# Performance work log

Measured on AMD Instinct MI355X. Metric: run time of the kernel, lower is better.

## Reference

```python
import jax, jax.numpy as jnp
import numpy as np

CUBE_SIZE = 24
N_NEURONS = CUBE_SIZE ** 3  # 13824
INPUT_DIM = 512
OUTPUT_DIM = 1000
MAX_STEPS = 30
BATCH = 256


def _build_neighbor_indices(size: int) -> np.ndarray:
    """[N, 27] int32; invalid (out-of-cube) neighbors map to pad slot N."""
    n = size ** 3
    c = np.arange(size)
    z, y, x = np.meshgrid(c, c, c, indexing='ij')  # each [size,size,size]
    cols = []
    for dz in (-1, 0, 1):
        for dy in (-1, 0, 1):
            for dx in (-1, 0, 1):
                nz, ny, nx = z + dz, y + dy, x + dx
                valid = ((nz >= 0) & (nz < size) & (ny >= 0) & (ny < size)
                         & (nx >= 0) & (nx < size))
                idx = nz * size * size + ny * size + nx
                cols.append(np.where(valid, idx, n))
    return np.stack(cols, axis=-1).reshape(n, 27).astype(np.int32)


def setup_inputs() -> dict:
    key = jax.random.key(0)
    ks = jax.random.split(key, 4)
    # xavier-ish small init scales (gain 0.5 style)
    w_in = jax.random.normal(ks[0], (N_NEURONS, INPUT_DIM), jnp.float32) * 0.01
    w_local = jax.random.normal(ks[1], (N_NEURONS, 27), jnp.float32) * 0.1
    w_out = jax.random.normal(ks[2], (OUTPUT_DIM, N_NEURONS), jnp.float32) * 0.01
    x = jax.random.normal(ks[3], (BATCH, INPUT_DIM), jnp.float32)
    return {
        'x': x,
        'W_in_w': w_in,
        'W_in_b': jnp.zeros((N_NEURONS,), jnp.float32),
        'W_local': w_local,
        'W_out_w': w_out,
        'W_out_b': jnp.zeros((OUTPUT_DIM,), jnp.float32),
        'neighbor_indices': jnp.asarray(_build_neighbor_indices(CUBE_SIZE)),
    }


def reference(x, W_in_w, W_in_b, W_local, W_out_w, W_out_b, neighbor_indices):
    batch = x.shape[0]
    x_proj = x @ W_in_w.T + W_in_b  # [B, N]
    h0 = jnp.zeros((batch, N_NEURONS), x.dtype)
    pad = jnp.zeros((batch, 1), x.dtype)

    def step(h, _):
        h_padded = jnp.concatenate([h, pad], axis=1)        # [B, N+1]
        nbr = h_padded[:, neighbor_indices]                  # [B, N, 27]
        weighted = jnp.einsum('bnk,nk->bn', nbr, W_local)    # [B, N]
        return jnp.tanh(x_proj + weighted), None

    h, _ = jax.lax.scan(step, h0, None, length=MAX_STEPS)
    return h @ W_out_w.T + W_out_b  # [B, output_dim]
```

## Files before the change

kernel.cpp:

```cpp
#include <hip/hip_runtime.h>
#include <hip/hip_bf16.h>

#define NN   13824
#define BB   256
#define KDIM 512
#define ODIM 1000
#define CUBE 24
#define KS   16
#define XSTR 516
#define OSTR 452

typedef short bf8 __attribute__((ext_vector_type(8)));
typedef float f32x4 __attribute__((ext_vector_type(4)));

__device__ __forceinline__ float fast_tanh(float a) {
    float e = __expf(2.0f * a);
    return 1.0f - 2.0f / (e + 1.0f);
}
__device__ __forceinline__ float bf_lo(unsigned u) { return __uint_as_float(u << 16); }
__device__ __forceinline__ float bf_hi(unsigned u) { return __uint_as_float(u & 0xffff0000u); }
__device__ __forceinline__ unsigned short bf_rne(float f) {
    unsigned u = __float_as_uint(f);
    u += 0x7fffu + ((u >> 16) & 1u);
    return (unsigned short)(u >> 16);
}
__device__ __forceinline__ unsigned pk_bf16(float lo, float hi) {
    union { __hip_bfloat162 h; unsigned u; } cv;
    cv.h = __float22bfloat162_rn(make_float2(lo, hi));
    return cv.u;
}

__global__ __launch_bounds__(256) void xbf_kernel(
    const float* __restrict__ x, unsigned* __restrict__ xb)
{
    int i = blockIdx.x * 256 + threadIdx.x;
    float2 v = *(const float2*)&x[(size_t)i * 2];
    xb[i] = pk_bf16(v.x, v.y);
}

__global__ __launch_bounds__(256) void xproj_mfma(
    const float* __restrict__ w_in, const float* __restrict__ bias,
    const short* __restrict__ xbf, unsigned short* __restrict__ xp,
    unsigned short* __restrict__ h1)
{
    __shared__ unsigned short As[16 * XSTR];
    const int tid = threadIdx.x, w = tid >> 6, lane = tid & 63;
    const int quad = lane >> 4, l16 = lane & 15;
    const int n0 = blockIdx.x * 16;

#pragma unroll
    for (int rr = 0; rr < 4; ++rr) {
        const int row = w * 4 + rr;
        const float* __restrict__ src = &w_in[(size_t)(n0 + row) * KDIM];
#pragma unroll
        for (int c = 0; c < 2; ++c) {
            const int col = c * 256 + lane * 4;
            float4 v = *(const float4*)&src[col];
            uint2 pk2 = make_uint2(pk_bf16(v.x, v.y), pk_bf16(v.z, v.w));
            *(uint2*)&As[row * XSTR + col] = pk2;
        }
    }
    __syncthreads();

    f32x4 acc[4] = {};

    int ka = quad * 8;
    bf8 bb[4];
#pragma unroll
    for (int j = 0; j < 4; ++j)
        bb[j] = *(const bf8*)&xbf[(size_t)(w * 64 + j * 16 + l16) * KDIM + ka];

    for (int it = 0; it < 16; ++it) {
        bf8 nb[4] = {};
        if (it < 15) {
            const int nka = ka + 32;
#pragma unroll
            for (int j = 0; j < 4; ++j)
                nb[j] = *(const bf8*)&xbf[(size_t)(w * 64 + j * 16 + l16) * KDIM + nka];
        }
        bf8 af = *(const bf8*)&As[l16 * XSTR + it * 32 + quad * 8];
#pragma unroll
        for (int j = 0; j < 4; ++j)
            acc[j] = __builtin_amdgcn_mfma_f32_16x16x32_bf16(af, bb[j], acc[j], 0, 0, 0);
#pragma unroll
        for (int j = 0; j < 4; ++j) bb[j] = nb[j];
        ka += 32;
    }

#pragma unroll
    for (int j = 0; j < 4; ++j) {
        const int b = w * 64 + j * 16 + l16;
#pragma unroll
        for (int r = 0; r < 4; ++r) {
            const int n = n0 + quad * 4 + r;
            const float v = acc[j][r] + bias[n];
            xp[(size_t)n * BB + b] = bf_rne(v);
            h1[(size_t)n * BB + b] = bf_rne(fast_tanh(v));
        }
    }
}

__device__ __forceinline__ void load_plane_f2(
    const unsigned* __restrict__ h32, int z, int y, int xx, int dof, float2* w9)
{
#pragma unroll
    for (int j = 0; j < 9; ++j) {
        const int dz = j / 3 - 1, dy = j % 3 - 1;
        const int zz = z + dz, yy = y + dy;
        const bool valid = (xx >= 0) & (xx < CUBE) & (zz >= 0) & (zz < CUBE) &
                           (yy >= 0) & (yy < CUBE);
        unsigned v = 0u;
        if (valid) v = h32[(size_t)((zz * 24 + yy) * 24 + xx) * 128 + dof];
        w9[j] = make_float2(bf_lo(v), bf_hi(v));
    }
}

__global__ __launch_bounds__(256) void step_kernel(
    const unsigned* __restrict__ hprev, const unsigned* __restrict__ xp,
    const float* __restrict__ wl, unsigned* __restrict__ hnext)
{
    const int tid  = threadIdx.x;
    const int wid  = __builtin_amdgcn_readfirstlane(tid >> 6);
    const int wvb  = wid & 1;
    const int yoff = wid >> 1;
    const int lane = tid & 63;

    const int bid   = blockIdx.x;
    const int zhi   = bid & 7;
    const int inner = bid >> 3;
    const int yp    = inner % 12;
    const int r     = inner / 12;
    const int xc    = r & 3;
    const int zlo   = r >> 2;
    const int z     = zhi * 3 + zlo;
    const int y     = yp * 2 + yoff;

    const int x0   = xc * 6;
    const int dof  = wvb * 64 + lane;

    float2 win[5][9];
    load_plane_f2(hprev, z, y, x0 - 1, dof, win[0]);
    load_plane_f2(hprev, z, y, x0,     dof, win[1]);
    load_plane_f2(hprev, z, y, x0 + 1, dof, win[2]);
    load_plane_f2(hprev, z, y, x0 + 2, dof, win[3]);

#pragma unroll
    for (int xi = 0; xi < 6; ++xi) {
        const int x = x0 + xi;
        if (xi <= 3)
            load_plane_f2(hprev, z, y, x + 3, dof, win[(xi + 4) % 5]);

        const int n = (z * 24 + y) * 24 + x;
        const float* __restrict__ wn = &wl[(size_t)n * 27];
        const unsigned xpv = xp[(size_t)n * 128 + dof];
        float2 acc = make_float2(bf_lo(xpv), bf_hi(xpv));

        const float2* pm = win[xi % 5];
        const float2* pc = win[(xi + 1) % 5];
        const float2* pp = win[(xi + 2) % 5];
#pragma unroll
        for (int j = 0; j < 9; ++j) {
            const float w0 = wn[3 * j + 0];
            const float w1 = wn[3 * j + 1];
            const float w2 = wn[3 * j + 2];
            acc.x += w0 * pm[j].x + w1 * pc[j].x + w2 * pp[j].x;
            acc.y += w0 * pm[j].y + w1 * pc[j].y + w2 * pp[j].y;
        }
        hnext[(size_t)n * 128 + dof] = pk_bf16(fast_tanh(acc.x), fast_tanh(acc.y));
    }
}

__global__ __launch_bounds__(256) void transpose_kernel(
    const unsigned* __restrict__ h32, unsigned* __restrict__ hT32)
{
    __shared__ unsigned short T[64][66];
    const int tid = threadIdx.x;
    const int rr = tid >> 2, g = tid & 3;
    const int k0 = blockIdx.x * 64, b0 = blockIdx.y * 64;
#pragma unroll
    for (int i = 0; i < 8; ++i) {
        unsigned d = h32[(size_t)(k0 + rr) * 128 + b0 / 2 + g * 8 + i];
        const int bl = (g * 8 + i) * 2;
        T[bl][rr]     = (unsigned short)(d & 0xffffu);
        T[bl + 1][rr] = (unsigned short)(d >> 16);
    }
    __syncthreads();
#pragma unroll
    for (int i = 0; i < 8; ++i) {
        const int kl = (g * 8 + i) * 2;
        unsigned d = (unsigned)T[rr][kl] | ((unsigned)T[rr][kl + 1] << 16);
        hT32[(size_t)(b0 + rr) * (NN / 2) + k0 / 2 + g * 8 + i] = d;
    }
}

__global__ __launch_bounds__(512) void outgemm_mfma(
    const float* __restrict__ wout, const short* __restrict__ hT,
    float* __restrict__ part)
{
    __shared__ unsigned short As[128 * OSTR];
    const int tid = threadIdx.x, w = tid >> 6, lane = tid & 63;
    const int quad = lane >> 4, l16 = lane & 15;
    const int kb = blockIdx.x * (NN / KS);
    const int o0 = blockIdx.y * 128;
    const int b0 = blockIdx.z * 128 + w * 16;

    f32x4 acc[8] = {};

#pragma unroll 1
    for (int ph = 0; ph < 2; ++ph) {
        const int poff  = ph ? 448 : 0;
        const int pcols = ph ? 416 : 448;
        const int pkc   = ph ? 13 : 14;
        if (ph) __syncthreads();

#pragma unroll 4
        for (int rr = 0; rr < 16; ++rr) {
            const int row = w * 16 + rr;
            const int o = o0 + row;
            const float* __restrict__ src = &wout[(size_t)o * NN + kb + poff];
#pragma unroll
            for (int c = 0; c < 2; ++c) {
                const int col = c * 256 + lane * 4;
                if (col < pcols) {
                    float4 v = {0.f, 0.f, 0.f, 0.f};
                    if (o < ODIM) v = *(const float4*)&src[col];
                    *(uint2*)&As[row * OSTR + col] =
                        make_uint2(pk_bf16(v.x, v.y), pk_bf16(v.z, v.w));
                }
            }
        }
        __syncthreads();

        bf8 bb;
        {
            const int ka = kb + poff + quad * 8;
            bb = *(const bf8*)&hT[(size_t)(b0 + l16) * NN + ka];
        }
        for (int kc = 0; kc < pkc; ++kc) {
            bf8 nb = {};
            if (kc + 1 < pkc) {
                const int ka = kb + poff + (kc + 1) * 32 + quad * 8;
                nb = *(const bf8*)&hT[(size_t)(b0 + l16) * NN + ka];
            }
            const int cs = kc * 32 + quad * 8;
#pragma unroll
            for (int t = 0; t < 8; ++t) {
                bf8 af = *(const bf8*)&As[(t * 16 + l16) * OSTR + cs];
                acc[t] = __builtin_amdgcn_mfma_f32_16x16x32_bf16(af, bb, acc[t], 0, 0, 0);
            }
            bb = nb;
        }
    }

#pragma unroll
    for (int t = 0; t < 8; ++t) {
        const int b = b0 + l16;
#pragma unroll
        for (int r = 0; r < 4; ++r) {
            const int o = o0 + t * 16 + quad * 4 + r;
            part[((size_t)blockIdx.x * 1024 + o) * BB + b] = acc[t][r];
        }
    }
}

__global__ __launch_bounds__(256) void reduce_kernel(
    const float* __restrict__ part, const float* __restrict__ bias,
    float* __restrict__ out)
{
    const int o = blockIdx.x, b = threadIdx.x;
    float s = bias[o];
#pragma unroll
    for (int kc = 0; kc < KS; ++kc)
        s += part[((size_t)kc * 1024 + o) * BB + b];
    out[(size_t)b * ODIM + o] = s;
}

extern "C" void kernel_launch(void* const* d_in, const int* in_sizes, int n_in,
                              void* d_out, int out_size, void* d_ws, size_t ws_size,
                              hipStream_t stream)
{
    const float* x       = (const float*)d_in[0];
    const float* w_in    = (const float*)d_in[1];
    const float* b_in    = (const float*)d_in[2];
    const float* w_local = (const float*)d_in[3];
    const float* w_out   = (const float*)d_in[4];
    const float* b_out   = (const float*)d_in[5];
    float* out = (float*)d_out;

    char* p = (char*)d_ws;
    unsigned short* xp_bf = (unsigned short*)p;          p += (size_t)NN * BB * 2;
    unsigned short* hA    = (unsigned short*)p;          p += (size_t)NN * BB * 2;
    unsigned short* hB    = (unsigned short*)p;          p += (size_t)NN * BB * 2;
    unsigned short* hT    = (unsigned short*)p;          p += (size_t)NN * BB * 2;
    unsigned short* x_bf  = (unsigned short*)p;          p += (size_t)BB * KDIM * 2;
    float*          part  = (float*)p;

    xbf_kernel<<<256, 256, 0, stream>>>(x, (unsigned*)x_bf);
    xproj_mfma<<<864, 256, 0, stream>>>(w_in, b_in, (const short*)x_bf, xp_bf, hA);

    const unsigned* hp = (const unsigned*)hA;
    unsigned* hn = (unsigned*)hB;
    for (int s = 0; s < 29; ++s) {
        step_kernel<<<1152, 256, 0, stream>>>(hp, (const unsigned*)xp_bf, w_local, hn);
        unsigned* t = (unsigned*)hp; hp = hn; hn = t;
    }

    transpose_kernel<<<dim3(216, 4), 256, 0, stream>>>(hp, (unsigned*)hT);
    outgemm_mfma<<<dim3(KS, 8, 2), 512, 0, stream>>>(w_out, (const short*)hT, part);
    reduce_kernel<<<ODIM, 256, 0, stream>>>(part, b_out, out);
}
```

Measured before the change: 547.3 us.

## Retile step kernel to 4-wide x strips and double-buffer outgemm B loads

The stencil step kernel changes its thread-block decomposition. Each wave now handles its own y row, each thread walks 4 x positions instead of 6, and the grid grows to 1728 blocks. The input-projection values for all 4 positions are loaded up front to hide latency. The output GEMM gets a two-deep prefetch of the B fragments so global loads overlap more MFMA work. The trade-off is more parallelism and occupancy against more redundant halo-plane loads per output, since 6 planes are loaded per 4 outputs instead of 8 per 6.

```diff
diff --git a/kernel.cpp b/kernel.cpp
--- a/kernel.cpp
+++ b/kernel.cpp
@@ -121,22 +121,23 @@
 {
     const int tid  = threadIdx.x;
     const int wid  = __builtin_amdgcn_readfirstlane(tid >> 6);
-    const int wvb  = wid & 1;
-    const int yoff = wid >> 1;
     const int lane = tid & 63;
 
     const int bid   = blockIdx.x;
     const int zhi   = bid & 7;
     const int inner = bid >> 3;
-    const int yp    = inner % 12;
-    const int r     = inner / 12;
-    const int xc    = r & 3;
-    const int zlo   = r >> 2;
+    const int half  = inner & 1;
+    const int u     = inner >> 1;
+    const int xc    = u % 6;
+    const int u2    = u / 6;
+    const int yq    = u2 % 6;
+    const int zlo   = u2 / 6;
     const int z     = zhi * 3 + zlo;
-    const int y     = yp * 2 + yoff;
-
-    const int x0   = xc * 6;
-    const int dof  = wvb * 64 + lane;
+    const int y     = yq * 4 + wid;
+
+    const int x0   = xc * 4;
+    const int dof  = half * 64 + lane;
+    const int n0   = (z * 24 + y) * 24 + x0;
 
     float2 win[5][9];
     load_plane_f2(hprev, z, y, x0 - 1, dof, win[0]);
@@ -144,16 +145,20 @@
     load_plane_f2(hprev, z, y, x0 + 1, dof, win[2]);
     load_plane_f2(hprev, z, y, x0 + 2, dof, win[3]);
 
-#pragma unroll
-    for (int xi = 0; xi < 6; ++xi) {
+    unsigned xpv[4];
+#pragma unroll
+    for (int xi = 0; xi < 4; ++xi)
+        xpv[xi] = xp[(size_t)(n0 + xi) * 128 + dof];
+
+#pragma unroll
+    for (int xi = 0; xi < 4; ++xi) {
         const int x = x0 + xi;
-        if (xi <= 3)
+        if (xi <= 1)
             load_plane_f2(hprev, z, y, x + 3, dof, win[(xi + 4) % 5]);
 
-        const int n = (z * 24 + y) * 24 + x;
+        const int n = n0 + xi;
         const float* __restrict__ wn = &wl[(size_t)n * 27];
-        const unsigned xpv = xp[(size_t)n * 128 + dof];
-        float2 acc = make_float2(bf_lo(xpv), bf_hi(xpv));
+        float2 acc = make_float2(bf_lo(xpv[xi]), bf_hi(xpv[xi]));
 
         const float2* pm = win[xi % 5];
         const float2* pc = win[(xi + 1) % 5];
@@ -203,6 +208,8 @@
     const int kb = blockIdx.x * (NN / KS);
     const int o0 = blockIdx.y * 128;
     const int b0 = blockIdx.z * 128 + w * 16;
+
+    const short* __restrict__ brow = &hT[(size_t)(b0 + l16) * NN];
 
     f32x4 acc[8] = {};
 
@@ -231,24 +238,31 @@
         }
         __syncthreads();
 
-        bf8 bb;
-        {
-            const int ka = kb + poff + quad * 8;
-            bb = *(const bf8*)&hT[(size_t)(b0 + l16) * NN + ka];
-        }
-        for (int kc = 0; kc < pkc; ++kc) {
-            bf8 nb = {};
+        const int kab = kb + poff + quad * 8;
+        bf8 s0 = *(const bf8*)&brow[kab];
+        bf8 s1 = *(const bf8*)&brow[kab + 32];
+
+        for (int kc = 0; kc < pkc; kc += 2) {
+            {
+                const int cs = kc * 32 + quad * 8;
+                bf8 cur = s0;
+                if (kc + 2 < pkc) s0 = *(const bf8*)&brow[kab + (kc + 2) * 32];
+#pragma unroll
+                for (int t = 0; t < 8; ++t) {
+                    bf8 af = *(const bf8*)&As[(t * 16 + l16) * OSTR + cs];
+                    acc[t] = __builtin_amdgcn_mfma_f32_16x16x32_bf16(af, cur, acc[t], 0, 0, 0);
+                }
+            }
             if (kc + 1 < pkc) {
-                const int ka = kb + poff + (kc + 1) * 32 + quad * 8;
-                nb = *(const bf8*)&hT[(size_t)(b0 + l16) * NN + ka];
+                const int cs = (kc + 1) * 32 + quad * 8;
+                bf8 cur = s1;
+                if (kc + 3 < pkc) s1 = *(const bf8*)&brow[kab + (kc + 3) * 32];
+#pragma unroll
+                for (int t = 0; t < 8; ++t) {
+                    bf8 af = *(const bf8*)&As[(t * 16 + l16) * OSTR + cs];
+                    acc[t] = __builtin_amdgcn_mfma_f32_16x16x32_bf16(af, cur, acc[t], 0, 0, 0);
+                }
             }
-            const int cs = kc * 32 + quad * 8;
-#pragma unroll
-            for (int t = 0; t < 8; ++t) {
-                bf8 af = *(const bf8*)&As[(t * 16 + l16) * OSTR + cs];
-                acc[t] = __builtin_amdgcn_mfma_f32_16x16x32_bf16(af, bb, acc[t], 0, 0, 0);
-            }
-            bb = nb;
         }
     }
 
@@ -301,7 +315,7 @@
     const unsigned* hp = (const unsigned*)hA;
     unsigned* hn = (unsigned*)hB;
     for (int s = 0; s < 29; ++s) {
-        step_kernel<<<1152, 256, 0, stream>>>(hp, (const unsigned*)xp_bf, w_local, hn);
+        step_kernel<<<1728, 256, 0, stream>>>(hp, (const unsigned*)xp_bf, w_local, hn);
         unsigned* t = (unsigned*)hp; hp = hn; hn = t;
     }
 
```

Result: no change. 537.3 us (-1.8%).
